# Performance work log

Hardware: AMD Instinct MI355X
Metric: run time of the kernel (lower is better)

Reference implementation:

```python
import jax, jax.numpy as jnp
import numpy as np

N = 3072        # nodes
NFEAT = 128
NHID = 64
NHEADS = 8
LENGTH = 8      # path length
NPATHS = 2048
NTASK = 4
ALPHA = 0.2     # LeakyReLU negative slope
NEG_INF = -9e15


def setup_inputs() -> dict:
    key = jax.random.key(0)
    ks = jax.random.split(key, 12)
    features = jax.random.normal(ks[0], (N, NFEAT), dtype=jnp.float32)
    adj = (jax.random.uniform(ks[1], (N, N)) < 0.01).astype(jnp.float32)
    adj = jnp.maximum(adj, jnp.eye(N, dtype=jnp.float32))
    path = jax.random.randint(ks[2], (NPATHS, LENGTH), 0, N)
    task = jax.random.randint(ks[3], (NPATHS * LENGTH,), 0, NTASK)
    s = 0.1
    Wp = jax.random.normal(ks[4], (NHEADS, NFEAT, NHID), dtype=jnp.float32) * s
    ap = jax.random.normal(ks[5], (NHEADS, 2 * NHID, 1), dtype=jnp.float32) * s
    Ws = jax.random.normal(ks[6], (NHEADS, NFEAT, NHID), dtype=jnp.float32) * s
    a_s = jax.random.normal(ks[7], (NHEADS, 2 * NHID, 1), dtype=jnp.float32) * s
    Wsc = jax.random.normal(ks[8], (NHID * NHEADS, NTASK), dtype=jnp.float32) * s
    bsc = jnp.zeros((NTASK,), dtype=jnp.float32)
    Wc = jax.random.normal(ks[9], (NHID * NHEADS * LENGTH * 2, 1), dtype=jnp.float32) * s
    bc = jnp.zeros((1,), dtype=jnp.float32)
    return dict(features=features, adj=adj, path=path, task=task,
                Wp=Wp, ap=ap, Ws=Ws, a_s=a_s, Wsc=Wsc, bsc=bsc, Wc=Wc, bc=bc)


def _gat_head(h, mask, W, a):
    # Dense GAT head: Wh [N,nhid]; e_ij = leakyrelu(a1.Wh_i + a2.Wh_j)
    Wh = h @ W                              # [N, nhid]
    f1 = Wh @ a[:NHID]                      # [N, 1]
    f2 = Wh @ a[NHID:]                      # [N, 1]
    e = jax.nn.leaky_relu(f1 + f2.T, negative_slope=ALPHA)  # [N, N]
    att = jax.nn.softmax(jnp.where(mask, e, NEG_INF), axis=1)
    return jax.nn.elu(att @ Wh)             # concat=True -> elu


def _multihead(h, mask, W, a):
    out = jax.vmap(_gat_head, in_axes=(None, None, 0, 0))(h, mask, W, a)  # [H,N,nhid]
    return jnp.transpose(out, (1, 0, 2)).reshape(h.shape[0], NHEADS * NHID)


def reference(features, adj, path, task, Wp, ap, Ws, a_s, Wsc, bsc, Wc, bc):
    mask = adj > 0
    private_x = _multihead(features, mask, Wp, ap)   # [N, H*nhid]
    share_x = _multihead(features, mask, Ws, a_s)    # [N, H*nhid]
    idx = path.reshape(-1)                           # [P*L]
    share_feature = share_x[idx]                     # [P*L, H*nhid]
    private_feature = private_x[idx]                 # [P*L, H*nhid]
    # adversarial task loss: cross_entropy(softmax(sigmoid(logits)), task)
    logits = share_feature @ Wsc + bsc
    node_task = jax.nn.softmax(jax.nn.sigmoid(logits), axis=1)
    logp = jax.nn.log_softmax(node_task, axis=1)
    adv_loss = -jnp.mean(jnp.take_along_axis(logp, task[:, None], axis=1))
    # diff loss: ||S^T P||_F^2
    diff = share_feature.T @ private_feature         # [H*nhid, H*nhid]
    diff_loss = jnp.sum(diff ** 2)
    x = jnp.concatenate([share_feature, private_feature], axis=1)
    x = x.reshape(-1, NHID * NHEADS * LENGTH * 2)    # [P, 8192]
    x = jax.nn.sigmoid(x @ Wc + bc)                  # [P, 1]
    return (x, adv_loss, diff_loss)
```

## Files before the change

### kernel.cpp

```cpp
#include <hip/hip_runtime.h>
#include <hip/hip_bf16.h>
#include <math.h>

#define NN     3072
#define NF     128
#define NHID   64
#define HEADS  8
#define LEN    8
#define NPATH  2048
#define NTK    4
#define NELEM  (NPATH*LEN)
#define MAXDEG 128
#define SH     16
#define KSPLIT 12
#define KCH    (NN / KSPLIT)
#define NDIFB  (KSPLIT * 64)
#define NADV   192
#define NDIF   256

__global__ void k_pre(const float* __restrict__ feat,
                      const float* __restrict__ Wp, const float* __restrict__ Ws,
                      const float* __restrict__ ap, const float* __restrict__ as_,
                      const float* __restrict__ adj,
                      float* __restrict__ whg, float* __restrict__ f1g,
                      float* __restrict__ f2g, int* __restrict__ cols,
                      int* __restrict__ cnt, int* __restrict__ hist,
                      int* __restrict__ histT, float* __restrict__ out) {
    __shared__ float Fs[32][68];
    __shared__ float Wsh[32][64];
    int b = blockIdx.x;
    int tid = threadIdx.x;
    if (b < 768) {
        int rt = b % 48, sh = b / 48;
        int set = sh >> 3, head = sh & 7;
        int g = sh >> 2, sg = sh & 3;
        const float* W = (set ? Ws : Wp) + (size_t)head * NF * NHID;
        const float* a = (set ? as_ : ap) + (size_t)head * 2 * NHID;
        int tc = (tid & 15) * 4;
        int tr = (tid >> 4) * 4;
        float acc[4][4] = {};
        for (int k0 = 0; k0 < NF; k0 += 32) {
            for (int i = tid; i < 512; i += 256) {
                int r = i >> 3, kq = (i & 7) * 4;
                float4 v = *(const float4*)&feat[(size_t)(rt * 64 + r) * NF + k0 + kq];
                Fs[kq + 0][r] = v.x; Fs[kq + 1][r] = v.y;
                Fs[kq + 2][r] = v.z; Fs[kq + 3][r] = v.w;
            }
            for (int i = tid; i < 512; i += 256) {
                int k = i >> 4, cq = (i & 15) * 4;
                *(float4*)&Wsh[k][cq] = *(const float4*)&W[(size_t)(k0 + k) * NHID + cq];
            }
            __syncthreads();
            #pragma unroll
            for (int k = 0; k < 32; ++k) {
                float4 av = *(const float4*)&Fs[k][tr];
                float4 bv = *(const float4*)&Wsh[k][tc];
                float a_[4] = {av.x, av.y, av.z, av.w};
                float b_[4] = {bv.x, bv.y, bv.z, bv.w};
                #pragma unroll
                for (int i = 0; i < 4; ++i)
                    #pragma unroll
                    for (int j = 0; j < 4; ++j) acc[i][j] += a_[i] * b_[j];
            }
            __syncthreads();
        }
        #pragma unroll
        for (int i = 0; i < 4; ++i)
            *(float4*)&whg[(((size_t)g * NN + rt * 64 + tr + i) * 4 + sg) * NHID + tc] =
                *(float4*)&acc[i][0];
        float4 a1 = *(const float4*)&a[tc];
        float4 a2 = *(const float4*)&a[NHID + tc];
        float p1[4], p2[4];
        #pragma unroll
        for (int i = 0; i < 4; ++i) {
            p1[i] = acc[i][0]*a1.x + acc[i][1]*a1.y + acc[i][2]*a1.z + acc[i][3]*a1.w;
            p2[i] = acc[i][0]*a2.x + acc[i][1]*a2.y + acc[i][2]*a2.z + acc[i][3]*a2.w;
        }
        #pragma unroll
        for (int o = 1; o < 16; o <<= 1) {
            #pragma unroll
            for (int i = 0; i < 4; ++i) {
                p1[i] += __shfl_xor(p1[i], o);
                p2[i] += __shfl_xor(p2[i], o);
            }
        }
        if ((tid & 15) == 0) {
            #pragma unroll
            for (int i = 0; i < 4; ++i) {
                f1g[((size_t)g * NN + rt * 64 + tr + i) * 4 + sg] = p1[i];
                f2g[((size_t)g * NN + rt * 64 + tr + i) * 4 + sg] = p2[i];
            }
        }
        return;
    }
    int cb = b - 768;
    if (cb < 64) {
        int i = cb * 256 + tid;
        if (i < NN) hist[i] = 0;
        if (i < NN * NTK) histT[i] = 0;
        if (i == 0) { out[NPATH] = 0.f; out[NPATH + 1] = 0.f; }
    }
    int row  = cb * 4 + (tid >> 6);
    int lane = tid & 63;
    const float* ar = adj + (size_t)row * NN;
    int* cr = cols + (size_t)row * MAXDEG;
    int base = 0;
    for (int c0 = 0; c0 < NN; c0 += 256) {
        float4 v = *(const float4*)&ar[c0 + lane * 4];
        float e[4] = {v.x, v.y, v.z, v.w};
        #pragma unroll
        for (int q = 0; q < 4; ++q) {
            bool pred = e[q] > 0.f;
            unsigned long long bb = __ballot(pred);
            int before = __popcll(bb & ((1ull << lane) - 1ull));
            if (pred && (base + before) < MAXDEG) cr[base + before] = c0 + lane * 4 + q;
            base += __popcll(bb);
        }
    }
    if (lane == 0) cnt[row] = base < MAXDEG ? base : MAXDEG;
}

__global__ void k_gat(const float* __restrict__ whg, const float* __restrict__ f1g,
                      const float* __restrict__ f2g, const int* __restrict__ cols,
                      const int* __restrict__ cnt, const int* __restrict__ path,
                      const int* __restrict__ task, int* __restrict__ hist,
                      int* __restrict__ histT, float* __restrict__ xo) {
    __shared__ float attT[4][MAXDEG][4];
    __shared__ int   cls[4][MAXDEG];
    int b = blockIdx.x;
    if (b < 64) {
        int i = b * 256 + threadIdx.x;
        int node = path[i];
        atomicAdd(&hist[node], 1);
        atomicAdd(&histT[node * NTK + task[i]], 1);
    }
    int g = (b & 7) >> 1;
    int node4 = ((b >> 3) << 1) | (b & 1);
    int w = threadIdx.x >> 6;
    int lane = threadIdx.x & 63;
    int node = node4 * 4 + w;
    int deg = cnt[node];
    const int* cl = cols + (size_t)node * MAXDEG;
    const float* f2p = f2g + (size_t)g * NN * 4;
    float4 f1q = *(const float4*)&f1g[((size_t)g * NN + node) * 4];
    float f1v[4] = {f1q.x, f1q.y, f1q.z, f1q.w};

    float e0[4], e1[4];
    #pragma unroll
    for (int t = 0; t < 2; ++t) {
        int l = lane + t * 64;
        bool valid = l < deg;
        int j = valid ? cl[l] : 0;
        if (valid) cls[w][l] = j;
        float4 q = *(const float4*)&f2p[(size_t)j * 4];
        float f2v[4] = {q.x, q.y, q.z, q.w};
        float* e = t ? e1 : e0;
        #pragma unroll
        for (int s = 0; s < 4; ++s) {
            float x = f1v[s] + f2v[s];
            x = (x >= 0.f) ? x : 0.2f * x;
            e[s] = valid ? x : -1e30f;
        }
    }
    float m[4], sl[4], inv[4];
    #pragma unroll
    for (int s = 0; s < 4; ++s) m[s] = fmaxf(e0[s], e1[s]);
    #pragma unroll
    for (int o = 32; o; o >>= 1)
        #pragma unroll
        for (int s = 0; s < 4; ++s) m[s] = fmaxf(m[s], __shfl_xor(m[s], o));
    float ex0[4], ex1[4];
    #pragma unroll
    for (int s = 0; s < 4; ++s) {
        ex0[s] = expf(e0[s] - m[s]);
        ex1[s] = expf(e1[s] - m[s]);
        sl[s] = ex0[s] + ex1[s];
    }
    #pragma unroll
    for (int o = 32; o; o >>= 1)
        #pragma unroll
        for (int s = 0; s < 4; ++s) sl[s] += __shfl_xor(sl[s], o);
    #pragma unroll
    for (int s = 0; s < 4; ++s) inv[s] = 1.f / sl[s];
    *(float4*)&attT[w][lane][0]      = make_float4(ex0[0], ex0[1], ex0[2], ex0[3]);
    *(float4*)&attT[w][lane + 64][0] = make_float4(ex1[0], ex1[1], ex1[2], ex1[3]);

    const float* base = whg + (size_t)g * NN * 256;
    float acc0 = 0.f, acc1 = 0.f, acc2 = 0.f, acc3 = 0.f;
    int l = 0;
    for (; l + 2 <= deg; l += 2) {
        int ja = cls[w][l], jb = cls[w][l + 1];
        const float* wa = base + (size_t)ja * 256 + lane;
        const float* wb = base + (size_t)jb * 256 + lane;
        float4 aa = *(const float4*)&attT[w][l][0];
        float4 ab = *(const float4*)&attT[w][l + 1][0];
        float va0 = wa[0], va1 = wa[64], va2 = wa[128], va3 = wa[192];
        float vb0 = wb[0], vb1 = wb[64], vb2 = wb[128], vb3 = wb[192];
        acc0 += aa.x * va0; acc1 += aa.y * va1; acc2 += aa.z * va2; acc3 += aa.w * va3;
        acc0 += ab.x * vb0; acc1 += ab.y * vb1; acc2 += ab.z * vb2; acc3 += ab.w * vb3;
    }
    if (l < deg) {
        int j = cls[w][l];
        const float* wr = base + (size_t)j * 256 + lane;
        float4 a4 = *(const float4*)&attT[w][l][0];
        acc0 += a4.x * wr[0];   acc1 += a4.y * wr[64];
        acc2 += a4.z * wr[128]; acc3 += a4.w * wr[192];
    }
    float accv[4] = {acc0, acc1, acc2, acc3};
    #pragma unroll
    for (int s = 0; s < 4; ++s) {
        float v = accv[s] * inv[s];
        v = (v > 0.f) ? v : (expf(v) - 1.f);
        int sh = g * 4 + s;
        int set = sh >> 3, head = sh & 7;
        xo[((size_t)set * NN + node) * (HEADS * NHID) + head * NHID + lane] = v;
    }
}

__global__ void k_diffadv(const float* __restrict__ S, const float* __restrict__ P,
                          const int* __restrict__ hist, const float* __restrict__ Wsc,
                          const float* __restrict__ bsc, const int* __restrict__ histT,
                          const float* __restrict__ Wc, float* __restrict__ Dp,
                          float* __restrict__ nodeDot, float* __restrict__ out) {
    __shared__ float4 shbuf[2176];
    float* As = (float*)shbuf;
    float* Bs = As + 64 * 68;
    int b = blockIdx.x;
    int tid = threadIdx.x;
    if (b < NADV) {
        int wave = tid >> 6;
        int lane = tid & 63;
        const float4* Wc4 = (const float4*)Wc;
        float sloc = 0.f;
        #pragma unroll
        for (int i = 0; i < 4; ++i) {
            int w = b * 16 + wave * 4 + i;
            const float* Srow = S + (size_t)w * 512;
            const float* Prow = P + (size_t)w * 512;
            float4 s0 = *(const float4*)&Srow[lane * 8];
            float4 s1 = *(const float4*)&Srow[lane * 8 + 4];
            float4 p0 = *(const float4*)&Prow[lane * 8];
            float4 p1 = *(const float4*)&Prow[lane * 8 + 4];
            float d[8];
            #pragma unroll
            for (int l = 0; l < 8; ++l) {
                float4 wS0 = Wc4[l * 256 + lane * 2];
                float4 wS1 = Wc4[l * 256 + lane * 2 + 1];
                float4 wP0 = Wc4[l * 256 + 128 + lane * 2];
                float4 wP1 = Wc4[l * 256 + 128 + lane * 2 + 1];
                d[l] = s0.x*wS0.x + s0.y*wS0.y + s0.z*wS0.z + s0.w*wS0.w
                     + s1.x*wS1.x + s1.y*wS1.y + s1.z*wS1.z + s1.w*wS1.w
                     + p0.x*wP0.x + p0.y*wP0.y + p0.z*wP0.z + p0.w*wP0.w
                     + p1.x*wP1.x + p1.y*wP1.y + p1.z*wP1.z + p1.w*wP1.w;
            }
            #pragma unroll
            for (int o = 32; o; o >>= 1)
                #pragma unroll
                for (int l = 0; l < 8; ++l) d[l] += __shfl_xor(d[l], o);
            if (lane == 0) {
                *(float4*)&nodeDot[(size_t)w * 8]     = make_float4(d[0], d[1], d[2], d[3]);
                *(float4*)&nodeDot[(size_t)w * 8 + 4] = make_float4(d[4], d[5], d[6], d[7]);
            }
            float vv[8] = {s0.x, s0.y, s0.z, s0.w, s1.x, s1.y, s1.z, s1.w};
            float p[4] = {0.f, 0.f, 0.f, 0.f};
            #pragma unroll
            for (int qq = 0; qq < 8; ++qq) {
                float4 wv = *(const float4*)&Wsc[(lane * 8 + qq) * 4];
                p[0] += vv[qq] * wv.x; p[1] += vv[qq] * wv.y;
                p[2] += vv[qq] * wv.z; p[3] += vv[qq] * wv.w;
            }
            for (int o = 32; o; o >>= 1) {
                p[0] += __shfl_xor(p[0], o); p[1] += __shfl_xor(p[1], o);
                p[2] += __shfl_xor(p[2], o); p[3] += __shfl_xor(p[3], o);
            }
            if (lane == 0) {
                float sg[4], mx = -1e30f;
                for (int j = 0; j < 4; ++j) {
                    sg[j] = 1.f / (1.f + expf(-(p[j] + bsc[j])));
                    mx = fmaxf(mx, sg[j]);
                }
                float ex[4], se = 0.f;
                for (int j = 0; j < 4; ++j) { ex[j] = expf(sg[j] - mx); se += ex[j]; }
                float pr[4], pe = 0.f;
                for (int j = 0; j < 4; ++j) { pr[j] = ex[j] / se; }
                for (int j = 0; j < 4; ++j) { pe += expf(pr[j]); }
                float lse = logf(pe);
                for (int j = 0; j < 4; ++j)
                    sloc += (float)histT[w * NTK + j] * (pr[j] - lse);
            }
        }
        if (lane == 0) As[wave] = sloc;
        __syncthreads();
        if (tid == 0) {
            float t = As[0] + As[1] + As[2] + As[3];
            if (t != 0.f) atomicAdd(&out[NPATH], -t * (1.f / (float)NELEM));
        }
        return;
    }
    int d_ = b - NADV;
    int z = d_ >> 6, rem = d_ & 63;
    int a0 = (rem >> 3) * 64, b0 = (rem & 7) * 64;
    int kbase = z * KCH;
    int tr = (tid >> 4) * 4, tc = (tid & 15) * 4;
    float acc[4][4] = {};
    for (int k0 = 0; k0 < KCH; k0 += 64) {
        for (int i = tid; i < 64 * 16; i += 256) {
            int k = i >> 4, c4 = (i & 15) * 4;
            int krow = kbase + k0 + k;
            float wgt = (float)hist[krow];
            float4 sv = *(const float4*)&S[(size_t)krow * 512 + a0 + c4];
            As[k * 68 + c4 + 0] = sv.x * wgt; As[k * 68 + c4 + 1] = sv.y * wgt;
            As[k * 68 + c4 + 2] = sv.z * wgt; As[k * 68 + c4 + 3] = sv.w * wgt;
            float4 pv = *(const float4*)&P[(size_t)krow * 512 + b0 + c4];
            Bs[k * 68 + c4 + 0] = pv.x; Bs[k * 68 + c4 + 1] = pv.y;
            Bs[k * 68 + c4 + 2] = pv.z; Bs[k * 68 + c4 + 3] = pv.w;
        }
        __syncthreads();
        #pragma unroll
        for (int k = 0; k < 64; ++k) {
            float4 av = *(const float4*)&As[k * 68 + tr];
            float4 bv = *(const float4*)&Bs[k * 68 + tc];
            float a_[4] = {av.x, av.y, av.z, av.w};
            float b_[4] = {bv.x, bv.y, bv.z, bv.w};
            #pragma unroll
            for (int i = 0; i < 4; ++i)
                #pragma unroll
                for (int j = 0; j < 4; ++j) acc[i][j] += a_[i] * b_[j];
        }
        __syncthreads();
    }
    float* dst = Dp + (size_t)z * 512 * 512;
    #pragma unroll
    for (int i = 0; i < 4; ++i)
        *(float4*)&dst[(size_t)(a0 + tr + i) * 512 + b0 + tc] = *(float4*)&acc[i][0];
}

__global__ void k_final(const int* __restrict__ path, const float* __restrict__ nodeDot,
                        const float* __restrict__ bc, const float* __restrict__ Dp,
                        float* __restrict__ out) {
    __shared__ float red[256];
    int b = blockIdx.x;
    int tid = threadIdx.x;
    if (b < 8) {
        int p = b * 256 + tid;
        float s = bc[0];
        #pragma unroll
        for (int l = 0; l < 8; ++l) {
            int node = path[p * LEN + l];
            s += nodeDot[(size_t)node * 8 + l];
        }
        out[p] = 1.f / (1.f + expf(-s));
        return;
    }
    int e4 = (b - 8) * 256 + tid;
    float4 a = {0.f, 0.f, 0.f, 0.f};
    for (int z = 0; z < KSPLIT; ++z) {
        float4 v = *(const float4*)&Dp[(size_t)z * 512 * 512 + (size_t)e4 * 4];
        a.x += v.x; a.y += v.y; a.z += v.z; a.w += v.w;
    }
    red[tid] = a.x * a.x + a.y * a.y + a.z * a.z + a.w * a.w;
    __syncthreads();
    for (int o = 128; o; o >>= 1) {
        if (tid < o) red[tid] += red[tid + o];
        __syncthreads();
    }
    if (tid == 0) atomicAdd(&out[NPATH + 1], red[0]);
}

extern "C" void kernel_launch(void* const* d_in, const int* in_sizes, int n_in,
                              void* d_out, int out_size, void* d_ws, size_t ws_size,
                              hipStream_t stream) {
    const float* feat = (const float*)d_in[0];
    const float* adj  = (const float*)d_in[1];
    const int*   path = (const int*)d_in[2];
    const int*   task = (const int*)d_in[3];
    const float* Wp   = (const float*)d_in[4];
    const float* ap   = (const float*)d_in[5];
    const float* Ws   = (const float*)d_in[6];
    const float* as_  = (const float*)d_in[7];
    const float* Wsc  = (const float*)d_in[8];
    const float* bsc  = (const float*)d_in[9];
    const float* Wc   = (const float*)d_in[10];
    const float* bc   = (const float*)d_in[11];
    float* out = (float*)d_out;

    float* whg    = (float*)d_ws;
    float* f1g    = whg + (size_t)NN * SH * NHID;
    float* f2g    = f1g + (size_t)NN * SH;
    float* xo     = f2g + (size_t)NN * SH;
    float* Dp     = xo + (size_t)2 * NN * 512;
    float* nodeDot= Dp + (size_t)KSPLIT * 512 * 512;
    int*   cols   = (int*)(nodeDot + (size_t)NN * 8);
    int*   cnt    = cols + (size_t)NN * MAXDEG;
    int*   hist   = cnt + NN;
    int*   histT  = hist + NN;

    float* Pm = xo;
    float* Sm = xo + (size_t)NN * 512;

    k_pre<<<1536, 256, 0, stream>>>(feat, Wp, Ws, ap, as_, adj,
                                    whg, f1g, f2g, cols, cnt, hist, histT, out);
    k_gat<<<NN, 256, 0, stream>>>(whg, f1g, f2g, cols, cnt, path, task, hist, histT, xo);
    k_diffadv<<<NADV + NDIFB, 256, 0, stream>>>(Sm, Pm, hist, Wsc, bsc, histT,
                                                Wc, Dp, nodeDot, out);
    k_final<<<8 + NDIF, 256, 0, stream>>>(path, nodeDot, bc, Dp, out);
}
```

Baseline: 88.16 us.

## Store Wh in bf16 interleaved layout and compute four heads per GEMM block

The projection GEMM in k_pre now computes four heads per block, reusing each feature tile across four weight tiles, and runs 192 GEMM blocks instead of 768. Wh is written as bf16 with the four heads of a group interleaved per column, so each k_gat lane reads one 8-byte load per neighbour instead of four strided fp32 loads, halving gather traffic. The cost is bf16 rounding of Wh before the attention aggregation, plus more registers and shared memory in the GEMM blocks, which may lower occupancy.

```diff
diff --git a/kernel.cpp b/kernel.cpp
--- a/kernel.cpp
+++ b/kernel.cpp
@@ -17,28 +17,42 @@
 #define NDIFB  (KSPLIT * 64)
 #define NADV   192
 #define NDIF   256
+#define NGEMM  192
+
+static __device__ __forceinline__ unsigned f2bf(float x) {
+    unsigned u = __float_as_uint(x);
+    return (u + 0x7fffu + ((u >> 16) & 1u)) >> 16;
+}
+static __device__ __forceinline__ unsigned pk(float a, float b) {
+    return f2bf(a) | (f2bf(b) << 16);
+}
 
 __global__ void k_pre(const float* __restrict__ feat,
                       const float* __restrict__ Wp, const float* __restrict__ Ws,
                       const float* __restrict__ ap, const float* __restrict__ as_,
                       const float* __restrict__ adj,
-                      float* __restrict__ whg, float* __restrict__ f1g,
+                      unsigned short* __restrict__ whg16, float* __restrict__ f1g,
                       float* __restrict__ f2g, int* __restrict__ cols,
                       int* __restrict__ cnt, int* __restrict__ hist,
                       int* __restrict__ histT, float* __restrict__ out) {
     __shared__ float Fs[32][68];
-    __shared__ float Wsh[32][64];
+    __shared__ float Wsh[4][32][64];
     int b = blockIdx.x;
     int tid = threadIdx.x;
-    if (b < 768) {
-        int rt = b % 48, sh = b / 48;
-        int set = sh >> 3, head = sh & 7;
-        int g = sh >> 2, sg = sh & 3;
-        const float* W = (set ? Ws : Wp) + (size_t)head * NF * NHID;
-        const float* a = (set ? as_ : ap) + (size_t)head * 2 * NHID;
+    if (b < NGEMM) {
+        int rt = b % 48, g = b / 48;
         int tc = (tid & 15) * 4;
         int tr = (tid >> 4) * 4;
-        float acc[4][4] = {};
+        float acc[4][4][4] = {};
+        const float* Wsg[4];
+        const float* asg[4];
+        #pragma unroll
+        for (int sg = 0; sg < 4; ++sg) {
+            int sh = g * 4 + sg;
+            int set = sh >> 3, head = sh & 7;
+            Wsg[sg] = (set ? Ws : Wp) + (size_t)head * NF * NHID;
+            asg[sg] = (set ? as_ : ap) + (size_t)head * 2 * NHID;
+        }
         for (int k0 = 0; k0 < NF; k0 += 32) {
             for (int i = tid; i < 512; i += 256) {
                 int r = i >> 3, kq = (i & 7) * 4;
@@ -46,54 +60,77 @@
                 Fs[kq + 0][r] = v.x; Fs[kq + 1][r] = v.y;
                 Fs[kq + 2][r] = v.z; Fs[kq + 3][r] = v.w;
             }
-            for (int i = tid; i < 512; i += 256) {
-                int k = i >> 4, cq = (i & 15) * 4;
-                *(float4*)&Wsh[k][cq] = *(const float4*)&W[(size_t)(k0 + k) * NHID + cq];
-            }
+            #pragma unroll
+            for (int sg = 0; sg < 4; ++sg)
+                for (int i = tid; i < 512; i += 256) {
+                    int k = i >> 4, cq = (i & 15) * 4;
+                    *(float4*)&Wsh[sg][k][cq] =
+                        *(const float4*)&Wsg[sg][(size_t)(k0 + k) * NHID + cq];
+                }
             __syncthreads();
-            #pragma unroll
+            #pragma unroll 4
             for (int k = 0; k < 32; ++k) {
                 float4 av = *(const float4*)&Fs[k][tr];
-                float4 bv = *(const float4*)&Wsh[k][tc];
                 float a_[4] = {av.x, av.y, av.z, av.w};
-                float b_[4] = {bv.x, bv.y, bv.z, bv.w};
                 #pragma unroll
-                for (int i = 0; i < 4; ++i)
+                for (int sg = 0; sg < 4; ++sg) {
+                    float4 bv = *(const float4*)&Wsh[sg][k][tc];
+                    float b_[4] = {bv.x, bv.y, bv.z, bv.w};
                     #pragma unroll
-                    for (int j = 0; j < 4; ++j) acc[i][j] += a_[i] * b_[j];
+                    for (int i = 0; i < 4; ++i)
+                        #pragma unroll
+                        for (int j = 0; j < 4; ++j) acc[sg][i][j] += a_[i] * b_[j];
+                }
             }
             __syncthreads();
         }
         #pragma unroll
-        for (int i = 0; i < 4; ++i)
-            *(float4*)&whg[(((size_t)g * NN + rt * 64 + tr + i) * 4 + sg) * NHID + tc] =
-                *(float4*)&acc[i][0];
-        float4 a1 = *(const float4*)&a[tc];
-        float4 a2 = *(const float4*)&a[NHID + tc];
-        float p1[4], p2[4];
-        #pragma unroll
         for (int i = 0; i < 4; ++i) {
-            p1[i] = acc[i][0]*a1.x + acc[i][1]*a1.y + acc[i][2]*a1.z + acc[i][3]*a1.w;
-            p2[i] = acc[i][0]*a2.x + acc[i][1]*a2.y + acc[i][2]*a2.z + acc[i][3]*a2.w;
-        }
-        #pragma unroll
-        for (int o = 1; o < 16; o <<= 1) {
+            int node = rt * 64 + tr + i;
+            uint4 w0, w1;
+            w0.x = pk(acc[0][i][0], acc[1][i][0]); w0.y = pk(acc[2][i][0], acc[3][i][0]);
+            w0.z = pk(acc[0][i][1], acc[1][i][1]); w0.w = pk(acc[2][i][1], acc[3][i][1]);
+            w1.x = pk(acc[0][i][2], acc[1][i][2]); w1.y = pk(acc[2][i][2], acc[3][i][2]);
+            w1.z = pk(acc[0][i][3], acc[1][i][3]); w1.w = pk(acc[2][i][3], acc[3][i][3]);
+            unsigned short* dst = &whg16[(((size_t)g * NN + node) * 64 + tc) * 4];
+            *(uint4*)dst = w0;
+            *(uint4*)(dst + 8) = w1;
+        }
+        float p1[4][4], p2[4][4];
+        #pragma unroll
+        for (int sg = 0; sg < 4; ++sg) {
+            float4 a1 = *(const float4*)&asg[sg][tc];
+            float4 a2 = *(const float4*)&asg[sg][NHID + tc];
             #pragma unroll
             for (int i = 0; i < 4; ++i) {
-                p1[i] += __shfl_xor(p1[i], o);
-                p2[i] += __shfl_xor(p2[i], o);
-            }
-        }
+                p1[sg][i] = acc[sg][i][0]*a1.x + acc[sg][i][1]*a1.y
+                          + acc[sg][i][2]*a1.z + acc[sg][i][3]*a1.w;
+                p2[sg][i] = acc[sg][i][0]*a2.x + acc[sg][i][1]*a2.y
+                          + acc[sg][i][2]*a2.z + acc[sg][i][3]*a2.w;
+            }
+        }
+        #pragma unroll
+        for (int o = 1; o < 16; o <<= 1)
+            #pragma unroll
+            for (int sg = 0; sg < 4; ++sg)
+                #pragma unroll
+                for (int i = 0; i < 4; ++i) {
+                    p1[sg][i] += __shfl_xor(p1[sg][i], o);
+                    p2[sg][i] += __shfl_xor(p2[sg][i], o);
+                }
         if ((tid & 15) == 0) {
             #pragma unroll
             for (int i = 0; i < 4; ++i) {
-                f1g[((size_t)g * NN + rt * 64 + tr + i) * 4 + sg] = p1[i];
-                f2g[((size_t)g * NN + rt * 64 + tr + i) * 4 + sg] = p2[i];
+                int node = rt * 64 + tr + i;
+                *(float4*)&f1g[((size_t)g * NN + node) * 4] =
+                    make_float4(p1[0][i], p1[1][i], p1[2][i], p1[3][i]);
+                *(float4*)&f2g[((size_t)g * NN + node) * 4] =
+                    make_float4(p2[0][i], p2[1][i], p2[2][i], p2[3][i]);
             }
         }
         return;
     }
-    int cb = b - 768;
+    int cb = b - NGEMM;
     if (cb < 64) {
         int i = cb * 256 + tid;
         if (i < NN) hist[i] = 0;
@@ -120,11 +157,12 @@
     if (lane == 0) cnt[row] = base < MAXDEG ? base : MAXDEG;
 }
 
-__global__ void k_gat(const float* __restrict__ whg, const float* __restrict__ f1g,
-                      const float* __restrict__ f2g, const int* __restrict__ cols,
-                      const int* __restrict__ cnt, const int* __restrict__ path,
-                      const int* __restrict__ task, int* __restrict__ hist,
-                      int* __restrict__ histT, float* __restrict__ xo) {
+__global__ void k_gat(const unsigned short* __restrict__ whg16,
+                      const float* __restrict__ f1g, const float* __restrict__ f2g,
+                      const int* __restrict__ cols, const int* __restrict__ cnt,
+                      const int* __restrict__ path, const int* __restrict__ task,
+                      int* __restrict__ hist, int* __restrict__ histT,
+                      float* __restrict__ xo) {
     __shared__ float attT[4][MAXDEG][4];
     __shared__ int   cls[4][MAXDEG];
     int b = blockIdx.x;
@@ -185,26 +223,32 @@
     *(float4*)&attT[w][lane][0]      = make_float4(ex0[0], ex0[1], ex0[2], ex0[3]);
     *(float4*)&attT[w][lane + 64][0] = make_float4(ex1[0], ex1[1], ex1[2], ex1[3]);
 
-    const float* base = whg + (size_t)g * NN * 256;
+    const unsigned short* base16 = whg16 + (size_t)g * NN * 256;
     float acc0 = 0.f, acc1 = 0.f, acc2 = 0.f, acc3 = 0.f;
     int l = 0;
     for (; l + 2 <= deg; l += 2) {
         int ja = cls[w][l], jb = cls[w][l + 1];
-        const float* wa = base + (size_t)ja * 256 + lane;
-        const float* wb = base + (size_t)jb * 256 + lane;
+        uint2 va = *(const uint2*)&base16[(size_t)ja * 256 + lane * 4];
+        uint2 vb = *(const uint2*)&base16[(size_t)jb * 256 + lane * 4];
         float4 aa = *(const float4*)&attT[w][l][0];
         float4 ab = *(const float4*)&attT[w][l + 1][0];
-        float va0 = wa[0], va1 = wa[64], va2 = wa[128], va3 = wa[192];
-        float vb0 = wb[0], vb1 = wb[64], vb2 = wb[128], vb3 = wb[192];
-        acc0 += aa.x * va0; acc1 += aa.y * va1; acc2 += aa.z * va2; acc3 += aa.w * va3;
-        acc0 += ab.x * vb0; acc1 += ab.y * vb1; acc2 += ab.z * vb2; acc3 += ab.w * vb3;
+        acc0 += aa.x * __uint_as_float(va.x << 16);
+        acc1 += aa.y * __uint_as_float(va.x & 0xffff0000u);
+        acc2 += aa.z * __uint_as_float(va.y << 16);
+        acc3 += aa.w * __uint_as_float(va.y & 0xffff0000u);
+        acc0 += ab.x * __uint_as_float(vb.x << 16);
+        acc1 += ab.y * __uint_as_float(vb.x & 0xffff0000u);
+        acc2 += ab.z * __uint_as_float(vb.y << 16);
+        acc3 += ab.w * __uint_as_float(vb.y & 0xffff0000u);
     }
     if (l < deg) {
         int j = cls[w][l];
-        const float* wr = base + (size_t)j * 256 + lane;
+        uint2 v = *(const uint2*)&base16[(size_t)j * 256 + lane * 4];
         float4 a4 = *(const float4*)&attT[w][l][0];
-        acc0 += a4.x * wr[0];   acc1 += a4.y * wr[64];
-        acc2 += a4.z * wr[128]; acc3 += a4.w * wr[192];
+        acc0 += a4.x * __uint_as_float(v.x << 16);
+        acc1 += a4.y * __uint_as_float(v.x & 0xffff0000u);
+        acc2 += a4.z * __uint_as_float(v.y << 16);
+        acc3 += a4.w * __uint_as_float(v.y & 0xffff0000u);
     }
     float accv[4] = {acc0, acc1, acc2, acc3};
     #pragma unroll
@@ -384,8 +428,8 @@
     const float* bc   = (const float*)d_in[11];
     float* out = (float*)d_out;
 
-    float* whg    = (float*)d_ws;
-    float* f1g    = whg + (size_t)NN * SH * NHID;
+    unsigned short* whg16 = (unsigned short*)d_ws;
+    float* f1g    = (float*)(whg16 + (size_t)NN * SH * NHID);
     float* f2g    = f1g + (size_t)NN * SH;
     float* xo     = f2g + (size_t)NN * SH;
     float* Dp     = xo + (size_t)2 * NN * 512;
@@ -398,9 +442,9 @@
     float* Pm = xo;
     float* Sm = xo + (size_t)NN * 512;
 
-    k_pre<<<1536, 256, 0, stream>>>(feat, Wp, Ws, ap, as_, adj,
-                                    whg, f1g, f2g, cols, cnt, hist, histT, out);
-    k_gat<<<NN, 256, 0, stream>>>(whg, f1g, f2g, cols, cnt, path, task, hist, histT, xo);
+    k_pre<<<NGEMM + 768, 256, 0, stream>>>(feat, Wp, Ws, ap, as_, adj,
+                                           whg16, f1g, f2g, cols, cnt, hist, histT, out);
+    k_gat<<<NN, 256, 0, stream>>>(whg16, f1g, f2g, cols, cnt, path, task, hist, histT, xo);
     k_diffadv<<<NADV + NDIFB, 256, 0, stream>>>(Sm, Pm, hist, Wsc, bsc, histT,
                                                 Wc, Dp, nodeDot, out);
     k_final<<<8 + NDIF, 256, 0, stream>>>(path, nodeDot, bc, Dp, out);
```

Measured after the change: 102.0 us. +15.7%, slower.

## Fuse final reduction and path output into diffadv via last-block counters

Applied to the files above, without the earlier changes.

Removes the separate k_final launch. The last block of each split-K tile group, detected with an atomic counter and threadfence, sums the partial Dp tiles and accumulates the squared norm. The last adv block computes the per-path sigmoid outputs. This saves one kernel launch and its serial tail, but adds atomics, fences, and a serialized reduction done inside the final blocks.

```diff
diff --git a/kernel.cpp b/kernel.cpp
--- a/kernel.cpp
+++ b/kernel.cpp
@@ -16,7 +16,6 @@
 #define KCH    (NN / KSPLIT)
 #define NDIFB  (KSPLIT * 64)
 #define NADV   192
-#define NDIF   256
 
 __global__ void k_pre(const float* __restrict__ feat,
                       const float* __restrict__ Wp, const float* __restrict__ Ws,
@@ -25,7 +24,8 @@
                       float* __restrict__ whg, float* __restrict__ f1g,
                       float* __restrict__ f2g, int* __restrict__ cols,
                       int* __restrict__ cnt, int* __restrict__ hist,
-                      int* __restrict__ histT, float* __restrict__ out) {
+                      int* __restrict__ histT, int* __restrict__ ctrD,
+                      int* __restrict__ ctrA, float* __restrict__ out) {
     __shared__ float Fs[32][68];
     __shared__ float Wsh[32][64];
     int b = blockIdx.x;
@@ -98,7 +98,8 @@
         int i = cb * 256 + tid;
         if (i < NN) hist[i] = 0;
         if (i < NN * NTK) histT[i] = 0;
-        if (i == 0) { out[NPATH] = 0.f; out[NPATH + 1] = 0.f; }
+        if (i < 64) ctrD[i] = 0;
+        if (i == 0) { ctrA[0] = 0; out[NPATH] = 0.f; out[NPATH + 1] = 0.f; }
     }
     int row  = cb * 4 + (tid >> 6);
     int lane = tid & 63;
@@ -220,9 +221,12 @@
 __global__ void k_diffadv(const float* __restrict__ S, const float* __restrict__ P,
                           const int* __restrict__ hist, const float* __restrict__ Wsc,
                           const float* __restrict__ bsc, const int* __restrict__ histT,
-                          const float* __restrict__ Wc, float* __restrict__ Dp,
-                          float* __restrict__ nodeDot, float* __restrict__ out) {
+                          const float* __restrict__ Wc, const int* __restrict__ path,
+                          const float* __restrict__ bc, float* __restrict__ Dp,
+                          float* __restrict__ nodeDot, int* __restrict__ ctrD,
+                          int* __restrict__ ctrA, float* __restrict__ out) {
     __shared__ float4 shbuf[2176];
+    __shared__ int flag;
     float* As = (float*)shbuf;
     float* Bs = As + 64 * 68;
     int b = blockIdx.x;
@@ -294,6 +298,21 @@
         if (tid == 0) {
             float t = As[0] + As[1] + As[2] + As[3];
             if (t != 0.f) atomicAdd(&out[NPATH], -t * (1.f / (float)NELEM));
+        }
+        __threadfence();
+        if (tid == 0) flag = (atomicAdd(ctrA, 1) == NADV - 1) ? 1 : 0;
+        __syncthreads();
+        if (!flag) return;
+        __threadfence();
+        float bias = bc[0];
+        for (int p = tid; p < NPATH; p += 256) {
+            float s = bias;
+            #pragma unroll
+            for (int l = 0; l < 8; ++l) {
+                int node = path[p * LEN + l];
+                s += nodeDot[(size_t)node * 8 + l];
+            }
+            out[p] = 1.f / (1.f + expf(-s));
         }
         return;
     }
@@ -333,32 +352,23 @@
     #pragma unroll
     for (int i = 0; i < 4; ++i)
         *(float4*)&dst[(size_t)(a0 + tr + i) * 512 + b0 + tc] = *(float4*)&acc[i][0];
-}
-
-__global__ void k_final(const int* __restrict__ path, const float* __restrict__ nodeDot,
-                        const float* __restrict__ bc, const float* __restrict__ Dp,
-                        float* __restrict__ out) {
-    __shared__ float red[256];
-    int b = blockIdx.x;
-    int tid = threadIdx.x;
-    if (b < 8) {
-        int p = b * 256 + tid;
-        float s = bc[0];
-        #pragma unroll
-        for (int l = 0; l < 8; ++l) {
-            int node = path[p * LEN + l];
-            s += nodeDot[(size_t)node * 8 + l];
-        }
-        out[p] = 1.f / (1.f + expf(-s));
-        return;
-    }
-    int e4 = (b - 8) * 256 + tid;
-    float4 a = {0.f, 0.f, 0.f, 0.f};
-    for (int z = 0; z < KSPLIT; ++z) {
-        float4 v = *(const float4*)&Dp[(size_t)z * 512 * 512 + (size_t)e4 * 4];
-        a.x += v.x; a.y += v.y; a.z += v.z; a.w += v.w;
-    }
-    red[tid] = a.x * a.x + a.y * a.y + a.z * a.z + a.w * a.w;
+    __threadfence();
+    if (tid == 0) flag = (atomicAdd(&ctrD[rem], 1) == KSPLIT - 1) ? 1 : 0;
+    __syncthreads();
+    if (!flag) return;
+    __threadfence();
+    float ssum = 0.f;
+    for (int e = tid; e < 4096; e += 256) {
+        int r = e >> 6, c = e & 63;
+        size_t off = (size_t)(a0 + r) * 512 + b0 + c;
+        float v = 0.f;
+        #pragma unroll
+        for (int z2 = 0; z2 < KSPLIT; ++z2)
+            v += Dp[(size_t)z2 * 512 * 512 + off];
+        ssum += v * v;
+    }
+    float* red = As;
+    red[tid] = ssum;
     __syncthreads();
     for (int o = 128; o; o >>= 1) {
         if (tid < o) red[tid] += red[tid + o];
@@ -394,14 +404,17 @@
     int*   cnt    = cols + (size_t)NN * MAXDEG;
     int*   hist   = cnt + NN;
     int*   histT  = hist + NN;
+    int*   ctrD   = histT + (size_t)NN * NTK;
+    int*   ctrA   = ctrD + 64;
 
     float* Pm = xo;
     float* Sm = xo + (size_t)NN * 512;
 
     k_pre<<<1536, 256, 0, stream>>>(feat, Wp, Ws, ap, as_, adj,
-                                    whg, f1g, f2g, cols, cnt, hist, histT, out);
+                                    whg, f1g, f2g, cols, cnt, hist, histT,
+                                    ctrD, ctrA, out);
     k_gat<<<NN, 256, 0, stream>>>(whg, f1g, f2g, cols, cnt, path, task, hist, histT, xo);
     k_diffadv<<<NADV + NDIFB, 256, 0, stream>>>(Sm, Pm, hist, Wsc, bsc, histT,
-                                                Wc, Dp, nodeDot, out);
-    k_final<<<8 + NDIF, 256, 0, stream>>>(path, nodeDot, bc, Dp, out);
+                                                Wc, path, bc, Dp, nodeDot,
+                                                ctrD, ctrA, out);
 }
```

Measured after the change: 197.5 us. +124.0%, slower.
